# Performance work log

Measured on AMD Instinct MI355X. Metric: run time of the kernel, lower is better.

## Reference

```python
import math
import jax, jax.numpy as jnp
import numpy as np

N = 100_000          # nodes
D = 128              # sample.num_node_features
E = 1_600_000        # edges (avg degree 16)
ACM = 4              # augmented_channels_multiplier
C = 128              # channels = 4*4*channels_optuna(=8)
RATIO = 0.7          # topk_ratio + 0.1
FINAL_NODES = 3


def setup_inputs() -> dict:
    key = jax.random.key(0)
    ks = jax.random.split(key, 14)
    s = 0.05
    x = jax.random.normal(ks[0], (N, D), jnp.float32)
    edge_index = jax.random.randint(ks[1], (2, E), 0, N, dtype=jnp.int32)
    # dense_input GraphConv(D, ACM): called with empty edges -> only lin_root weight + lin_rel bias matter
    Wd_root = jax.random.normal(ks[2], (ACM, D), jnp.float32) * s
    bd = jax.random.normal(ks[3], (ACM,), jnp.float32) * s
    # input GraphConv(ACM, C)
    Wi_rel = jax.random.normal(ks[4], (C, ACM), jnp.float32) * s
    bi = jax.random.normal(ks[5], (C,), jnp.float32) * s
    Wi_root = jax.random.normal(ks[6], (C, ACM), jnp.float32) * s
    # TopKPooling(C) attention vector
    p = jax.random.normal(ks[7], (C,), jnp.float32) * s
    # conv1 GraphConv(C, 2C)
    W1_rel = jax.random.normal(ks[8], (2 * C, C), jnp.float32) * s
    b1 = jax.random.normal(ks[9], (2 * C,), jnp.float32) * s
    W1_root = jax.random.normal(ks[10], (2 * C, C), jnp.float32) * s
    # output Linear(3 * 2C, 1)
    Wo = jax.random.normal(ks[11], (1, FINAL_NODES * 2 * C), jnp.float32) * s
    bo = jax.random.normal(ks[12], (1,), jnp.float32) * s
    return {"x": x, "edge_index": edge_index, "Wd_root": Wd_root, "bd": bd,
            "Wi_rel": Wi_rel, "bi": bi, "Wi_root": Wi_root, "p": p,
            "W1_rel": W1_rel, "b1": b1, "W1_root": W1_root, "Wo": Wo, "bo": bo}


def reference(x, edge_index, Wd_root, bd, Wi_rel, bi, Wi_root, p, W1_rel, b1, W1_root, Wo, bo):
    n = x.shape[0]
    src, dst = edge_index[0], edge_index[1]  # messages flow src -> dst

    # dense_input GraphConv with empty edge set: aggr == 0 -> lin_rel bias + lin_root(x)
    h = jax.nn.gelu(x @ Wd_root.T + bd, approximate=False)               # [N, ACM]

    # input GraphConv(ACM, C): out = lin_rel(sum_j x_j) + lin_root(x)
    aggr = jax.ops.segment_sum(h[src], dst, num_segments=n)              # [N, ACM]
    h = jax.nn.gelu(aggr @ Wi_rel.T + bi + h @ Wi_root.T, approximate=False)  # [N, C]

    # TopKPooling(C, ratio=0.7): score = tanh(x.p / ||p||), keep top-k, scale kept x by score
    k = int(math.ceil(RATIO * n))
    score = jnp.tanh((h @ p) / jnp.linalg.norm(p))                        # [N]
    top_scores, perm = jax.lax.top_k(score, k)
    hp = h[perm] * top_scores[:, None]                                    # [k, C]
    # remap edges: kept node -> new index, dropped -> sentinel k
    inv = jnp.full((n,), k, dtype=jnp.int32).at[perm].set(jnp.arange(k, dtype=jnp.int32))
    ns, nd = inv[src], inv[dst]
    valid = (ns < k) & (nd < k)

    # conv1 GraphConv(C, 2C) on coarsened graph (masked scatter, sentinel row dropped)
    msg = jnp.where(valid[:, None], hp[jnp.minimum(ns, k - 1)], 0.0)      # [E, C]
    aggr = jax.ops.segment_sum(msg, jnp.where(valid, nd, k), num_segments=k + 1)[:k]
    h2 = jax.nn.gelu(aggr @ W1_rel.T + b1 + hp @ W1_root.T, approximate=False)  # [k, 2C]

    # avg_pool_x with cluster = i % 3 over single-graph batch
    cluster = jnp.arange(k, dtype=jnp.int32) % FINAL_NODES
    sums = jax.ops.segment_sum(h2, cluster, num_segments=FINAL_NODES)
    counts = jax.ops.segment_sum(jnp.ones((k,), h2.dtype), cluster, num_segments=FINAL_NODES)
    pooled = sums / counts[:, None]                                       # [3, 2C]

    # output Linear on flattened vector -> shape [1]
    return pooled.reshape(-1) @ Wo.T + bo
```

## Files before the change

kernel.cpp:

```cpp
#include <hip/hip_runtime.h>
#include <stdint.h>

#define N_NODES 100000
#define D_FEAT  128
#define E_EDGES 1600000
#define ACMC    4
#define CCH     128
#define C2CH    256
#define KKEEP   70000
#define KPAD    70016
#define NBLK    547
#define BINCAP  64
#define NBINS   (1 << 20)
#define NWIN    8
#define WWIN    12500

typedef unsigned int u32;
typedef unsigned long long u64;
typedef unsigned short u16;
typedef short bf16x8 __attribute__((ext_vector_type(8)));
typedef float f32x4 __attribute__((ext_vector_type(4)));
typedef int i32x4 __attribute__((ext_vector_type(4)));

__device__ __forceinline__ float gelu_exact(float v){
    return 0.5f * v * (1.0f + erff(v * 0.70710678118654752440f));
}
__device__ __forceinline__ float bflo(u32 v){ return __uint_as_float(v << 16); }
__device__ __forceinline__ float bfhi(u32 v){ return __uint_as_float(v & 0xFFFF0000u); }
__device__ __forceinline__ u16 f2bf(float f){
    u32 x = __float_as_uint(f);
    return (u16)((x + 0x7FFFu + ((x >> 16) & 1u)) >> 16);
}

__global__ __launch_bounds__(256) void k_build(const int* __restrict__ ei,
                                               int* __restrict__ deg,
                                               int* __restrict__ slot) {
    int b = blockIdx.x;
    int win = b & (NWIN - 1);
    int chunk = b >> 3;
    int e0 = (chunk * 256 + threadIdx.x) * 4;
    if (e0 >= E_EDGES) return;
    i32x4 dv = __builtin_nontemporal_load((const i32x4*)(ei + E_EDGES + e0));
    i32x4 sv = __builtin_nontemporal_load((const i32x4*)(ei + e0));
    int lo = win * WWIN, hi = lo + WWIN;
    #pragma unroll
    for (int j = 0; j < 4; j++) {
        int d = dv[j];
        if (d >= lo && d < hi) {
            int pos = atomicAdd(&deg[d], 1);
            if (pos < BINCAP) slot[d * BINCAP + pos] = sv[j];
        }
    }
}

__global__ __launch_bounds__(256) void k_h1(const float* __restrict__ x,
                                            const float* __restrict__ Wd,
                                            const float* __restrict__ bd,
                                            float* __restrict__ h1) {
    int tid = threadIdx.x;
    int wid = tid >> 6, lane = tid & 63;
    int node = blockIdx.x * 4 + wid;
    if (node >= N_NODES) return;
    const float2* xr = (const float2*)(x + (size_t)node * D_FEAT);
    float2 v = xr[lane];
    const float2* wd = (const float2*)Wd;
    float s[4];
    #pragma unroll
    for (int j = 0; j < 4; j++) {
        float2 w = wd[j * 64 + lane];
        s[j] = v.x * w.x + v.y * w.y;
    }
    #pragma unroll
    for (int off = 32; off > 0; off >>= 1) {
        #pragma unroll
        for (int j = 0; j < 4; j++) s[j] += __shfl_xor(s[j], off);
    }
    if (lane == 0) {
        float4 o;
        o.x = gelu_exact(s[0] + bd[0]);
        o.y = gelu_exact(s[1] + bd[1]);
        o.z = gelu_exact(s[2] + bd[2]);
        o.w = gelu_exact(s[3] + bd[3]);
        ((float4*)h1)[node] = o;
    }
}

__global__ __launch_bounds__(256) void k_aggr1g(const int* __restrict__ deg,
                                                const int* __restrict__ slot,
                                                const float* __restrict__ h1,
                                                float* __restrict__ aggr1) {
    int d = blockIdx.x * blockDim.x + threadIdx.x;
    if (d >= N_NODES) return;
    int cnt = deg[d]; if (cnt > BINCAP) cnt = BINCAP;
    int base = d * BINCAP;
    float4 acc = make_float4(0.f, 0.f, 0.f, 0.f);
    for (int i0 = 0; i0 < cnt; i0 += 8) {
        int m = cnt - i0; if (m > 8) m = 8;
        int ss[8];
        #pragma unroll
        for (int j = 0; j < 8; j++) {
            int sj = slot[base + i0 + j];
            ss[j] = (j < m) ? sj : 0;
        }
        float4 vv[8];
        #pragma unroll
        for (int j = 0; j < 8; j++) vv[j] = ((const float4*)h1)[ss[j]];
        #pragma unroll
        for (int j = 0; j < 8; j++) {
            float msk = (j < m) ? 1.f : 0.f;
            acc.x += msk * vv[j].x;
            acc.y += msk * vv[j].y;
            acc.z += msk * vv[j].z;
            acc.w += msk * vv[j].w;
        }
    }
    ((float4*)aggr1)[d] = acc;
}

__global__ __launch_bounds__(128) void k_h_score(const float* __restrict__ aggr1,
                                                 const float* __restrict__ h1,
                                                 const float* __restrict__ Wi_rel,
                                                 const float* __restrict__ bi,
                                                 const float* __restrict__ Wi_root,
                                                 const float* __restrict__ p,
                                                 u16* __restrict__ hsb,
                                                 u32* __restrict__ dkey,
                                                 int* __restrict__ hist) {
    int node = blockIdx.x;
    int c = threadIdx.x;
    float4 ag = ((const float4*)aggr1)[node];
    float4 hv = ((const float4*)h1)[node];
    float4 wr = ((const float4*)Wi_rel)[c];
    float4 wo = ((const float4*)Wi_root)[c];
    float val = ag.x * wr.x + ag.y * wr.y + ag.z * wr.z + ag.w * wr.w
              + hv.x * wo.x + hv.y * wo.y + hv.z * wo.z + hv.w * wo.w
              + bi[c];
    float g = gelu_exact(val);
    float pc = p[c];
    float hp = g * pc, pp = pc * pc;
    #pragma unroll
    for (int off = 32; off > 0; off >>= 1) {
        hp += __shfl_xor(hp, off);
        pp += __shfl_xor(pp, off);
    }
    __shared__ float sh[2], sp[2];
    __shared__ float sscore;
    int wid = c >> 6, lane = c & 63;
    if (lane == 0) { sh[wid] = hp; sp[wid] = pp; }
    __syncthreads();
    if (c == 0) {
        float H = sh[0] + sh[1], P = sp[0] + sp[1];
        float sc = tanhf(H / sqrtf(P));
        sscore = sc;
        u32 u = __float_as_uint(sc);
        u32 asc = (u & 0x80000000u) ? ~u : (u | 0x80000000u);
        u32 d = ~asc;
        dkey[node] = d;
        atomicAdd(&hist[d >> 12], 1);
    }
    __syncthreads();
    hsb[(size_t)node * CCH + c] = f2bf(g * sscore);
}

__global__ __launch_bounds__(1024) void k_scan1(const int* __restrict__ hist,
                                                int* __restrict__ cursor,
                                                int* __restrict__ bsum) {
    __shared__ int s[1024];
    int t = threadIdx.x;
    int g = blockIdx.x * 1024 + t;
    int v = hist[g];
    s[t] = v;
    __syncthreads();
    #pragma unroll
    for (int off = 1; off < 1024; off <<= 1) {
        int o = (t >= off) ? s[t - off] : 0;
        __syncthreads();
        s[t] += o;
        __syncthreads();
    }
    cursor[g] = s[t] - v;
    if (t == 1023) bsum[blockIdx.x] = s[t];
}

__global__ __launch_bounds__(1024) void k_scan2(int* __restrict__ bsum) {
    __shared__ int s[1024];
    int t = threadIdx.x;
    int v = bsum[t];
    s[t] = v;
    __syncthreads();
    #pragma unroll
    for (int off = 1; off < 1024; off <<= 1) {
        int o = (t >= off) ? s[t - off] : 0;
        __syncthreads();
        s[t] += o;
        __syncthreads();
    }
    bsum[t] = s[t] - v;
}

__global__ __launch_bounds__(1024) void k_scan3(int* __restrict__ cursor,
                                                const int* __restrict__ bsum) {
    int t = threadIdx.x;
    int g = blockIdx.x * 1024 + t;
    cursor[g] += bsum[blockIdx.x];
}

__global__ __launch_bounds__(256) void k_scatter(const u32* __restrict__ dkey,
                                                 int* __restrict__ cursor,
                                                 u64* __restrict__ out64) {
    int i = blockIdx.x * blockDim.x + threadIdx.x;
    if (i >= N_NODES) return;
    u32 d = dkey[i];
    int pos = atomicAdd(&cursor[d >> 12], 1);
    out64[pos] = (((u64)d) << 32) | (u32)i;
}

__global__ __launch_bounds__(256) void k_refine(const u64* __restrict__ out64,
                                                const int* __restrict__ cursor,
                                                const int* __restrict__ hist,
                                                int* __restrict__ rank,
                                                int* __restrict__ noder) {
    int pp = blockIdx.x * blockDim.x + threadIdx.x;
    if (pp >= N_NODES) return;
    u64 kp = out64[pp];
    u32 b = (u32)(kp >> 44);
    int end = cursor[b];
    int cnt = hist[b];
    int start = end - cnt;
    int r = start;
    if (cnt > 1) {
        int c = 0;
        for (int q = start; q < end; q++) c += (out64[q] < kp) ? 1 : 0;
        r = start + c;
    }
    int node = (int)(u32)kp;
    rank[node] = r;
    noder[r] = node;
}

__global__ __launch_bounds__(256) void k_gather(const int* __restrict__ deg,
                                                const int* __restrict__ slot,
                                                const int* __restrict__ rank,
                                                const u32* __restrict__ hsb32,
                                                u32* __restrict__ inb32) {
    int tid = threadIdx.x;
    int wid = tid >> 6, lane = tid & 63;
    int d = blockIdx.x * 4 + wid;
    if (d >= N_NODES) return;
    int rd = rank[d];
    if (rd >= KKEEP) return;
    int cnt = deg[d]; if (cnt > BINCAP) cnt = BINCAP;
    int base = d * BINCAP;
    float ax = 0.f, ay = 0.f;
    for (int i0 = 0; i0 < cnt; i0 += 16) {
        int m = cnt - i0; if (m > 16) m = 16;
        int ss[16];
        #pragma unroll
        for (int j = 0; j < 16; j++) {
            int sj = slot[base + i0 + j];
            ss[j] = (j < m) ? sj : 0;
        }
        int rr[16];
        u32 vv[16];
        #pragma unroll
        for (int j = 0; j < 16; j++) {
            rr[j] = rank[ss[j]];
            vv[j] = hsb32[(size_t)ss[j] * 64 + lane];
        }
        #pragma unroll
        for (int j = 0; j < 16; j++) {
            float msk = (j < m && rr[j] < KKEEP) ? 1.f : 0.f;
            ax += msk * bflo(vv[j]);
            ay += msk * bfhi(vv[j]);
        }
    }
    inb32[(size_t)rd * 128 + lane] = (u32)f2bf(ax) | ((u32)f2bf(ay) << 16);
}

__global__ __launch_bounds__(256) void k_pack(const int* __restrict__ noder,
                                              const u32* __restrict__ hsb32,
                                              u32* __restrict__ inb32) {
    int tid = threadIdx.x;
    int wave = tid >> 6, lane = tid & 63;
    int r = blockIdx.x * 4 + wave;
    if (r >= KPAD) return;
    if (r < KKEEP) {
        int n = noder[r];
        inb32[(size_t)r * 128 + 64 + lane] = hsb32[(size_t)n * 64 + lane];
    } else {
        inb32[(size_t)r * 128 + lane] = 0;
        inb32[(size_t)r * 128 + 64 + lane] = 0;
    }
}

__global__ __launch_bounds__(128) void k_wconv(const float* __restrict__ Wrel,
                                               const float* __restrict__ Wroot,
                                               u16* __restrict__ wcat) {
    int ch = blockIdx.x, t = threadIdx.x;
    wcat[(size_t)ch * 256 + t]       = f2bf(Wrel[(size_t)ch * 128 + t]);
    wcat[(size_t)ch * 256 + 128 + t] = f2bf(Wroot[(size_t)ch * 128 + t]);
}

__global__ __launch_bounds__(512, 2) void k_h2mfma(const u16* __restrict__ inb,
                                                   const u16* __restrict__ wcat,
                                                   const float* __restrict__ b1,
                                                   float* __restrict__ partial) {
    __shared__ u16 bs[256 * 256];
    __shared__ float ps[768];
    int tid = threadIdx.x;
    int blk = blockIdx.x;

    {
        int ch = tid >> 1;
        int seg = tid & 1;
        const char* src = (const char*)wcat + (size_t)ch * 512 + seg * 256;
        char* dst = (char*)bs + (size_t)ch * 512;
        int swz = (ch & 7) << 4;
        #pragma unroll
        for (int i = 0; i < 16; i++) {
            int k = seg * 256 + i * 16;
            *(i32x4*)(dst + (k ^ swz)) = *(const i32x4*)(src + i * 16);
        }
    }
    for (int i = tid; i < 768; i += 512) ps[i] = 0.f;
    __syncthreads();

    int lane = tid & 63, wave = tid >> 6;
    int wm = wave >> 1, wn = wave & 1;
    int col = lane & 15, quad = lane >> 4;
    int rbase = blk * 128 + wm * 32;
    int chbase = wn * 128;

    bf16x8 a[2][8];
    #pragma unroll
    for (int m = 0; m < 2; m++) {
        const char* ar = (const char*)inb + (size_t)(rbase + m * 16 + col) * 512 + quad * 16;
        #pragma unroll
        for (int k0 = 0; k0 < 8; k0++)
            a[m][k0] = *(const bf16x8*)(ar + k0 * 64);
    }

    f32x4 acc[2][8];
    #pragma unroll
    for (int m = 0; m < 2; m++)
        #pragma unroll
        for (int n = 0; n < 8; n++)
            acc[m][n] = (f32x4){0.f, 0.f, 0.f, 0.f};

    int swzr = (col & 7) << 4;
    #pragma unroll
    for (int k0 = 0; k0 < 8; k0++) {
        int kb = k0 * 64 + quad * 16;
        bf16x8 b[8];
        #pragma unroll
        for (int n = 0; n < 8; n++) {
            int ch = chbase + n * 16 + col;
            b[n] = *(const bf16x8*)((const char*)bs + (size_t)ch * 512 + (kb ^ swzr));
        }
        #pragma unroll
        for (int n = 0; n < 8; n++) {
            acc[0][n] = __builtin_amdgcn_mfma_f32_16x16x32_bf16(a[0][k0], b[n], acc[0][n], 0, 0, 0);
            acc[1][n] = __builtin_amdgcn_mfma_f32_16x16x32_bf16(a[1][k0], b[n], acc[1][n], 0, 0, 0);
        }
    }

    #pragma unroll
    for (int m = 0; m < 2; m++) {
        #pragma unroll
        for (int n = 0; n < 8; n++) {
            int ch = chbase + n * 16 + col;
            float bias = b1[ch];
            float p0 = 0.f, p1 = 0.f, p2 = 0.f;
            #pragma unroll
            for (int reg = 0; reg < 4; reg++) {
                int r = rbase + m * 16 + quad * 4 + reg;
                float g = (r < KKEEP) ? gelu_exact(acc[m][n][reg] + bias) : 0.f;
                int md = r % 3;
                if (md == 0) p0 += g; else if (md == 1) p1 += g; else p2 += g;
            }
            p0 += __shfl_xor(p0, 16); p0 += __shfl_xor(p0, 32);
            p1 += __shfl_xor(p1, 16); p1 += __shfl_xor(p1, 32);
            p2 += __shfl_xor(p2, 16); p2 += __shfl_xor(p2, 32);
            if (quad == 0) {
                atomicAdd(&ps[0 * 256 + ch], p0);
                atomicAdd(&ps[1 * 256 + ch], p1);
                atomicAdd(&ps[2 * 256 + ch], p2);
            }
        }
    }
    __syncthreads();
    for (int i = tid; i < 768; i += 512)
        partial[(size_t)blk * 768 + i] = ps[i];
}

__global__ __launch_bounds__(64) void k_poolred(const float* __restrict__ partial,
                                                float* __restrict__ pooled) {
    int j = blockIdx.x;
    int lane = threadIdx.x;
    float s = 0.f;
    for (int i = lane; i < NBLK; i += 64)
        s += partial[(size_t)i * 768 + j];
    #pragma unroll
    for (int off = 32; off > 0; off >>= 1) s += __shfl_xor(s, off);
    if (lane == 0) pooled[j] = s;
}

__global__ __launch_bounds__(768) void k_out(const float* __restrict__ pooled,
                                             const float* __restrict__ Wo,
                                             const float* __restrict__ bo,
                                             float* __restrict__ out) {
    __shared__ float red[12];
    int t = threadIdx.x;
    int ci = t >> 8;
    float cnt = (ci == 0) ? 23334.0f : 23333.0f;
    float acc = (pooled[t] / cnt) * Wo[t];
    #pragma unroll
    for (int off = 32; off > 0; off >>= 1) acc += __shfl_xor(acc, off);
    int wid = t >> 6, lane = t & 63;
    if (lane == 0) red[wid] = acc;
    __syncthreads();
    if (t == 0) {
        float s = 0.0f;
        #pragma unroll
        for (int w = 0; w < 12; w++) s += red[w];
        out[0] = s + bo[0];
    }
}

extern "C" void kernel_launch(void* const* d_in, const int* in_sizes, int n_in,
                              void* d_out, int out_size, void* d_ws, size_t ws_size,
                              hipStream_t stream) {
    const float* x       = (const float*)d_in[0];
    const int*   ei      = (const int*)d_in[1];
    const float* Wd      = (const float*)d_in[2];
    const float* bd      = (const float*)d_in[3];
    const float* Wi_rel  = (const float*)d_in[4];
    const float* bi      = (const float*)d_in[5];
    const float* Wi_root = (const float*)d_in[6];
    const float* p       = (const float*)d_in[7];
    const float* W1_rel  = (const float*)d_in[8];
    const float* b1      = (const float*)d_in[9];
    const float* W1_root = (const float*)d_in[10];
    const float* Wo      = (const float*)d_in[11];
    const float* bo      = (const float*)d_in[12];

    char* ws = (char*)d_ws;
    size_t off_b = 0;
    auto alloc = [&](size_t bytes) -> void* {
        void* ptr = ws + off_b;
        off_b += (bytes + 255) & ~(size_t)255;
        return ptr;
    };
    float* h1     = (float*)alloc((size_t)N_NODES * 4 * sizeof(float));
    float* aggr1  = (float*)alloc((size_t)N_NODES * 4 * sizeof(float));
    u16*   hsb    = (u16*)alloc((size_t)N_NODES * CCH * sizeof(u16));
    u32*   dkey   = (u32*)alloc((size_t)N_NODES * sizeof(u32));
    int*   rank   = (int*)alloc((size_t)N_NODES * sizeof(int));
    int*   noder  = (int*)alloc((size_t)N_NODES * sizeof(int));
    int*   deg    = (int*)alloc((size_t)N_NODES * sizeof(int));
    int*   slot   = (int*)alloc((size_t)N_NODES * BINCAP * sizeof(int));
    u16*   inb    = (u16*)alloc((size_t)KPAD * C2CH * sizeof(u16));
    u16*   wcat   = (u16*)alloc((size_t)C2CH * 256 * sizeof(u16));
    float* partial= (float*)alloc((size_t)NBLK * 768 * sizeof(float));
    float* pooled = (float*)alloc(768 * sizeof(float));
    (void)ws_size; (void)in_sizes; (void)n_in; (void)out_size;

    int* hist   = (int*)inb;
    int* cursor = (int*)inb + NBINS;
    u64* out64  = (u64*)((int*)inb + 2 * NBINS);
    int* bsum   = (int*)(out64 + N_NODES);

    hipMemsetAsync(deg, 0, (size_t)N_NODES * sizeof(int), stream);
    hipMemsetAsync(hist, 0, (size_t)NBINS * sizeof(int), stream);

    k_build<<<1563 * NWIN, 256, 0, stream>>>(ei, deg, slot);
    k_wconv<<<256, 128, 0, stream>>>(W1_rel, W1_root, wcat);

    k_h1<<<N_NODES / 4, 256, 0, stream>>>(x, Wd, bd, h1);
    k_aggr1g<<<(N_NODES + 255) / 256, 256, 0, stream>>>(deg, slot, h1, aggr1);
    k_h_score<<<N_NODES, 128, 0, stream>>>(aggr1, h1, Wi_rel, bi, Wi_root, p,
                                           hsb, dkey, hist);

    k_scan1<<<NBINS / 1024, 1024, 0, stream>>>(hist, cursor, bsum);
    k_scan2<<<1, 1024, 0, stream>>>(bsum);
    k_scan3<<<NBINS / 1024, 1024, 0, stream>>>(cursor, bsum);
    k_scatter<<<(N_NODES + 255) / 256, 256, 0, stream>>>(dkey, cursor, out64);
    k_refine<<<(N_NODES + 255) / 256, 256, 0, stream>>>(out64, cursor, hist, rank, noder);

    k_gather<<<(N_NODES + 3) / 4, 256, 0, stream>>>(deg, slot, rank,
                                                    (const u32*)hsb, (u32*)inb);
    k_pack<<<(KPAD + 3) / 4, 256, 0, stream>>>(noder, (const u32*)hsb, (u32*)inb);
    k_h2mfma<<<NBLK, 512, 0, stream>>>(inb, wcat, b1, partial);
    k_poolred<<<768, 64, 0, stream>>>(partial, pooled);
    k_out<<<1, 768, 0, stream>>>(pooled, Wo, bo, (float*)d_out);
}
```

Baseline: 437.2 us.

## Fuse front-end kernels into one launch and make score kernel persistent

Merges the edge-binning, first dense layer and weight-conversion kernels into a single launch that branches on block index, so the independent stages can overlap and fewer launches are issued. The score kernel becomes a grid-stride persistent kernel handling two nodes per 256-thread block. It stages the small weight vectors in shared memory and computes the norm of p once per block instead of once per node. The fused launch mixes atomic-heavy and bandwidth-heavy blocks, and the persistent loop adds three block barriers per iteration.

```diff
diff --git a/kernel.cpp b/kernel.cpp
--- a/kernel.cpp
+++ b/kernel.cpp
@@ -15,6 +15,11 @@
 #define NWIN    8
 #define WWIN    12500
 
+#define NB_BUILD (1563 * NWIN)
+#define NB_H1    (N_NODES / 4)
+#define NB_WCONV 128
+#define NB_FRONT (NB_BUILD + NB_H1 + NB_WCONV)
+
 typedef unsigned int u32;
 typedef unsigned long long u64;
 typedef unsigned short u16;
@@ -32,56 +37,68 @@
     return (u16)((x + 0x7FFFu + ((x >> 16) & 1u)) >> 16);
 }
 
-__global__ __launch_bounds__(256) void k_build(const int* __restrict__ ei,
+__global__ __launch_bounds__(256) void k_front(const int* __restrict__ ei,
                                                int* __restrict__ deg,
-                                               int* __restrict__ slot) {
+                                               int* __restrict__ slot,
+                                               const float* __restrict__ x,
+                                               const float* __restrict__ Wd,
+                                               const float* __restrict__ bd,
+                                               float* __restrict__ h1,
+                                               const float* __restrict__ Wrel,
+                                               const float* __restrict__ Wroot,
+                                               u16* __restrict__ wcat) {
     int b = blockIdx.x;
-    int win = b & (NWIN - 1);
-    int chunk = b >> 3;
-    int e0 = (chunk * 256 + threadIdx.x) * 4;
-    if (e0 >= E_EDGES) return;
-    i32x4 dv = __builtin_nontemporal_load((const i32x4*)(ei + E_EDGES + e0));
-    i32x4 sv = __builtin_nontemporal_load((const i32x4*)(ei + e0));
-    int lo = win * WWIN, hi = lo + WWIN;
-    #pragma unroll
-    for (int j = 0; j < 4; j++) {
-        int d = dv[j];
-        if (d >= lo && d < hi) {
-            int pos = atomicAdd(&deg[d], 1);
-            if (pos < BINCAP) slot[d * BINCAP + pos] = sv[j];
-        }
-    }
-}
-
-__global__ __launch_bounds__(256) void k_h1(const float* __restrict__ x,
-                                            const float* __restrict__ Wd,
-                                            const float* __restrict__ bd,
-                                            float* __restrict__ h1) {
-    int tid = threadIdx.x;
-    int wid = tid >> 6, lane = tid & 63;
-    int node = blockIdx.x * 4 + wid;
-    if (node >= N_NODES) return;
-    const float2* xr = (const float2*)(x + (size_t)node * D_FEAT);
-    float2 v = xr[lane];
-    const float2* wd = (const float2*)Wd;
-    float s[4];
-    #pragma unroll
-    for (int j = 0; j < 4; j++) {
-        float2 w = wd[j * 64 + lane];
-        s[j] = v.x * w.x + v.y * w.y;
-    }
-    #pragma unroll
-    for (int off = 32; off > 0; off >>= 1) {
-        #pragma unroll
-        for (int j = 0; j < 4; j++) s[j] += __shfl_xor(s[j], off);
-    }
-    if (lane == 0) {
-        float4 o;
-        o.x = gelu_exact(s[0] + bd[0]);
-        o.y = gelu_exact(s[1] + bd[1]);
-        o.z = gelu_exact(s[2] + bd[2]);
-        o.w = gelu_exact(s[3] + bd[3]);
-        ((float4*)h1)[node] = o;
+    if (b < NB_BUILD) {
+        int win = b & (NWIN - 1);
+        int chunk = b >> 3;
+        int e0 = (chunk * 256 + threadIdx.x) * 4;
+        if (e0 >= E_EDGES) return;
+        i32x4 dv = __builtin_nontemporal_load((const i32x4*)(ei + E_EDGES + e0));
+        i32x4 sv = __builtin_nontemporal_load((const i32x4*)(ei + e0));
+        int lo = win * WWIN, hi = lo + WWIN;
+        #pragma unroll
+        for (int j = 0; j < 4; j++) {
+            int d = dv[j];
+            if (d >= lo && d < hi) {
+                int pos = atomicAdd(&deg[d], 1);
+                if (pos < BINCAP) slot[d * BINCAP + pos] = sv[j];
+            }
+        }
+        return;
+    }
+    if (b < NB_BUILD + NB_H1) {
+        int tid = threadIdx.x;
+        int wid = tid >> 6, lane = tid & 63;
+        int node = (b - NB_BUILD) * 4 + wid;
+        const float2* xr = (const float2*)(x + (size_t)node * D_FEAT);
+        float2 v = xr[lane];
+        const float2* wd = (const float2*)Wd;
+        float s[4];
+        #pragma unroll
+        for (int j = 0; j < 4; j++) {
+            float2 w = wd[j * 64 + lane];
+            s[j] = v.x * w.x + v.y * w.y;
+        }
+        #pragma unroll
+        for (int off = 32; off > 0; off >>= 1) {
+            #pragma unroll
+            for (int j = 0; j < 4; j++) s[j] += __shfl_xor(s[j], off);
+        }
+        if (lane == 0) {
+            float4 o;
+            o.x = gelu_exact(s[0] + bd[0]);
+            o.y = gelu_exact(s[1] + bd[1]);
+            o.z = gelu_exact(s[2] + bd[2]);
+            o.w = gelu_exact(s[3] + bd[3]);
+            ((float4*)h1)[node] = o;
+        }
+        return;
+    }
+    {
+        int g = (b - NB_BUILD - NB_H1) * 256 + threadIdx.x;
+        int ch = g >> 7, t = g & 127;
+        wcat[(size_t)ch * 256 + t]       = f2bf(Wrel[(size_t)ch * 128 + t]);
+        wcat[(size_t)ch * 256 + 128 + t] = f2bf(Wroot[(size_t)ch * 128 + t]);
     }
 }
 
@@ -117,7 +134,7 @@
     ((float4*)aggr1)[d] = acc;
 }
 
-__global__ __launch_bounds__(128) void k_h_score(const float* __restrict__ aggr1,
+__global__ __launch_bounds__(256) void k_h_score(const float* __restrict__ aggr1,
                                                  const float* __restrict__ h1,
                                                  const float* __restrict__ Wi_rel,
                                                  const float* __restrict__ bi,
@@ -126,40 +143,61 @@
                                                  u16* __restrict__ hsb,
                                                  u32* __restrict__ dkey,
                                                  int* __restrict__ hist) {
-    int node = blockIdx.x;
-    int c = threadIdx.x;
-    float4 ag = ((const float4*)aggr1)[node];
-    float4 hv = ((const float4*)h1)[node];
-    float4 wr = ((const float4*)Wi_rel)[c];
-    float4 wo = ((const float4*)Wi_root)[c];
-    float val = ag.x * wr.x + ag.y * wr.y + ag.z * wr.z + ag.w * wr.w
-              + hv.x * wo.x + hv.y * wo.y + hv.z * wo.z + hv.w * wo.w
-              + bi[c];
-    float g = gelu_exact(val);
-    float pc = p[c];
-    float hp = g * pc, pp = pc * pc;
-    #pragma unroll
-    for (int off = 32; off > 0; off >>= 1) {
-        hp += __shfl_xor(hp, off);
-        pp += __shfl_xor(pp, off);
-    }
-    __shared__ float sh[2], sp[2];
-    __shared__ float sscore;
-    int wid = c >> 6, lane = c & 63;
-    if (lane == 0) { sh[wid] = hp; sp[wid] = pp; }
-    __syncthreads();
-    if (c == 0) {
-        float H = sh[0] + sh[1], P = sp[0] + sp[1];
-        float sc = tanhf(H / sqrtf(P));
-        sscore = sc;
-        u32 u = __float_as_uint(sc);
-        u32 asc = (u & 0x80000000u) ? ~u : (u | 0x80000000u);
-        u32 d = ~asc;
-        dkey[node] = d;
-        atomicAdd(&hist[d >> 12], 1);
-    }
-    __syncthreads();
-    hsb[(size_t)node * CCH + c] = f2bf(g * sscore);
+    __shared__ float4 swr[128], swo[128];
+    __shared__ float sbi[128], spv[128];
+    __shared__ float spred[2];
+    __shared__ float red[2][2];
+    __shared__ float sscore[2];
+    int tid = threadIdx.x;
+    if (tid < 128) {
+        swr[tid] = ((const float4*)Wi_rel)[tid];
+        swo[tid] = ((const float4*)Wi_root)[tid];
+        sbi[tid] = bi[tid];
+        spv[tid] = p[tid];
+    }
+    __syncthreads();
+    if (tid < 128) {
+        float pp = spv[tid] * spv[tid];
+        #pragma unroll
+        for (int off = 32; off > 0; off >>= 1) pp += __shfl_xor(pp, off);
+        if ((tid & 63) == 0) spred[tid >> 6] = pp;
+    }
+    __syncthreads();
+    float pnorm = sqrtf(spred[0] + spred[1]);
+
+    int half = tid >> 7;
+    int c = tid & 127;
+    int wih = (tid >> 6) & 1;
+    int lane = tid & 63;
+    float4 wr = swr[c], wo = swo[c];
+    float bic = sbi[c], pc = spv[c];
+
+    for (int node = blockIdx.x * 2 + half; node < N_NODES; node += gridDim.x * 2) {
+        float4 ag = ((const float4*)aggr1)[node];
+        float4 hv = ((const float4*)h1)[node];
+        float val = ag.x * wr.x + ag.y * wr.y + ag.z * wr.z + ag.w * wr.w
+                  + hv.x * wo.x + hv.y * wo.y + hv.z * wo.z + hv.w * wo.w
+                  + bic;
+        float g = gelu_exact(val);
+        float hp = g * pc;
+        #pragma unroll
+        for (int off = 32; off > 0; off >>= 1) hp += __shfl_xor(hp, off);
+        if (lane == 0) red[half][wih] = hp;
+        __syncthreads();
+        if (c == 0) {
+            float H = red[half][0] + red[half][1];
+            float sc = tanhf(H / pnorm);
+            sscore[half] = sc;
+            u32 u = __float_as_uint(sc);
+            u32 asc = (u & 0x80000000u) ? ~u : (u | 0x80000000u);
+            u32 d = ~asc;
+            dkey[node] = d;
+            atomicAdd(&hist[d >> 12], 1);
+        }
+        __syncthreads();
+        hsb[(size_t)node * CCH + c] = f2bf(g * sscore[half]);
+        __syncthreads();
+    }
 }
 
 __global__ __launch_bounds__(1024) void k_scan1(const int* __restrict__ hist,
@@ -291,14 +329,6 @@
         inb32[(size_t)r * 128 + lane] = 0;
         inb32[(size_t)r * 128 + 64 + lane] = 0;
     }
-}
-
-__global__ __launch_bounds__(128) void k_wconv(const float* __restrict__ Wrel,
-                                               const float* __restrict__ Wroot,
-                                               u16* __restrict__ wcat) {
-    int ch = blockIdx.x, t = threadIdx.x;
-    wcat[(size_t)ch * 256 + t]       = f2bf(Wrel[(size_t)ch * 128 + t]);
-    wcat[(size_t)ch * 256 + 128 + t] = f2bf(Wroot[(size_t)ch * 128 + t]);
 }
 
 __global__ __launch_bounds__(512, 2) void k_h2mfma(const u16* __restrict__ inb,
@@ -473,13 +503,12 @@
     hipMemsetAsync(deg, 0, (size_t)N_NODES * sizeof(int), stream);
     hipMemsetAsync(hist, 0, (size_t)NBINS * sizeof(int), stream);
 
-    k_build<<<1563 * NWIN, 256, 0, stream>>>(ei, deg, slot);
-    k_wconv<<<256, 128, 0, stream>>>(W1_rel, W1_root, wcat);
-
-    k_h1<<<N_NODES / 4, 256, 0, stream>>>(x, Wd, bd, h1);
+    k_front<<<NB_FRONT, 256, 0, stream>>>(ei, deg, slot, x, Wd, bd, h1,
+                                          W1_rel, W1_root, wcat);
+
     k_aggr1g<<<(N_NODES + 255) / 256, 256, 0, stream>>>(deg, slot, h1, aggr1);
-    k_h_score<<<N_NODES, 128, 0, stream>>>(aggr1, h1, Wi_rel, bi, Wi_root, p,
-                                           hsb, dkey, hist);
+    k_h_score<<<2048, 256, 0, stream>>>(aggr1, h1, Wi_rel, bi, Wi_root, p,
+                                        hsb, dkey, hist);
 
     k_scan1<<<NBINS / 1024, 1024, 0, stream>>>(hist, cursor, bsum);
     k_scan2<<<1, 1024, 0, stream>>>(bsum);
```

Result: faster. 415.9 us (-4.9%).
